# Kernel tuning notes

Hardware: AMD Instinct MI355X
Metric: run time of the kernel (lower is better)

Reference implementation:

```python
import jax, jax.numpy as jnp
import numpy as np

B, T, H, O, P, L = 128, 64, 512, 47, 4, 3
G = 4 * H


def setup_inputs() -> dict:
    key = jax.random.key(0)
    k = jax.random.split(key, 10)
    s = 0.05
    return {
        "x": jax.random.randint(k[0], (B, T), 0, O),
        "properties": jax.random.normal(k[1], (B, P), jnp.float32),
        "enc_w": jax.random.normal(k[2], (H, O), jnp.float32) * s,
        "enc_b": jnp.zeros((H,), jnp.float32),
        "dec_w": jax.random.normal(k[3], (O, H), jnp.float32) * s,
        "dec_b": jnp.zeros((O,), jnp.float32),
        "w_ih0": jax.random.normal(k[4], (G, H + P), jnp.float32) * s,
        "w_hh0": jax.random.normal(k[5], (G, H), jnp.float32) * s,
        "b_ih0": jnp.zeros((G,), jnp.float32).at[H:2 * H].set(1.0),
        "b_hh0": jnp.zeros((G,), jnp.float32).at[H:2 * H].set(1.0),
        "w_ih_rest": jax.random.normal(k[6], (L - 1, G, H), jnp.float32) * s,
        "w_hh_rest": jax.random.normal(k[7], (L - 1, G, H), jnp.float32) * s,
        "b_ih_rest": jnp.zeros((L - 1, G), jnp.float32).at[:, H:2 * H].set(1.0),
        "b_hh_rest": jnp.zeros((L - 1, G), jnp.float32).at[:, H:2 * H].set(1.0),
    }


def _lstm_cell(x, h, c, w_ih, w_hh, b_ih, b_hh):
    # torch gate order: i, f, g, o
    g = x @ w_ih.T + h @ w_hh.T + (b_ih + b_hh)
    i, f, gg, o = jnp.split(g, 4, axis=-1)
    c = jax.nn.sigmoid(f) * c + jax.nn.sigmoid(i) * jnp.tanh(gg)
    h = jax.nn.sigmoid(o) * jnp.tanh(c)
    return h, c


def reference(x, properties, enc_w, enc_b, dec_w, dec_b,
              w_ih0, w_hh0, b_ih0, b_hh0,
              w_ih_rest, w_hh_rest, b_ih_rest, b_hh_rest):
    batch = properties.shape[0]
    max_len = x.shape[1]
    n_layers = w_ih_rest.shape[0] + 1
    hidden = w_hh0.shape[1]
    out_size = dec_w.shape[0]

    # initial one-hot on symbol 1 (start token), encoded
    init = jnp.zeros((batch, out_size), properties.dtype).at[:, 1].set(1.0)
    inputs0 = init @ enc_w.T + enc_b  # [B, H]
    h0 = jnp.zeros((n_layers, batch, hidden), properties.dtype)
    c0 = jnp.zeros_like(h0)

    def step(carry, _):
        h, c, inp = carry
        xcat = jnp.concatenate([inp, properties], axis=1)  # [B, H+P]
        hs, cs = [], []
        hh, cc = _lstm_cell(xcat, h[0], c[0], w_ih0, w_hh0, b_ih0, b_hh0)
        hs.append(hh); cs.append(cc)
        for l in range(n_layers - 1):
            hh, cc = _lstm_cell(hh, h[l + 1], c[l + 1],
                                w_ih_rest[l], w_hh_rest[l],
                                b_ih_rest[l], b_hh_rest[l])
            hs.append(hh); cs.append(cc)
        logits = hh @ dec_w.T + dec_b          # [B, O]
        nxt = logits @ enc_w.T + enc_b         # feed logits back through encoder
        return (jnp.stack(hs), jnp.stack(cs), nxt), logits

    _, logits_seq = jax.lax.scan(step, (h0, c0, inputs0), None, length=max_len)
    return jnp.transpose(logits_seq, (1, 0, 2))  # [B, T, O]
```

## Files before the change

### kernel.cpp

```cpp
#include <hip/hip_runtime.h>
#include <hip/hip_fp16.h>
#include <math.h>

#define B 128
#define T 64
#define H 512
#define O 47
#define PP 4
#define G 2048
#define GH (G*H)
#define HB (H*B)


typedef _Float16 h16;
typedef _Float16 h16x2 __attribute__((ext_vector_type(2)));

__device__ __forceinline__ unsigned int pack2h(float a, float b) {
    union { unsigned int u; h16 h[2]; } c;
    c.h[0] = (h16)a; c.h[1] = (h16)b;
    return c.u;
}
__device__ __forceinline__ h16x2 as_h2(unsigned int u) {
    union { unsigned int u; h16x2 v; } c; c.u = u; return c.v;
}
__device__ __forceinline__ uint2 cload_u2(const unsigned int* p) {
    unsigned long long v = __hip_atomic_load((const unsigned long long*)p,
                                             __ATOMIC_RELAXED, __HIP_MEMORY_SCOPE_AGENT);
    union { unsigned long long u; uint2 w; } c; c.u = v; return c.w;
}
__device__ __forceinline__ void cstore_u2(unsigned int* p, uint2 v) {
    union { unsigned long long u; uint2 w; } c; c.w = v;
    __hip_atomic_store((unsigned long long*)p, c.u,
                       __ATOMIC_RELAXED, __HIP_MEMORY_SCOPE_AGENT);
}
#define FDOT2(w, x, c) __builtin_amdgcn_fdot2(as_h2(w), as_h2(x), (c), false)

#define SM_WH     0
#define SM_BIAS   12288
#define SM_DECH   14336
#define SM_BL     14592
#define SM_G      14608
#define SM_DB     22800
#define SM_H      23824
#define SM_TOTAL  24080

struct RnnParams {
  const float* w_hh0;
  const float* w_ihr;
  const float* w_hhr;
  const float* b_ihr;
  const float* b_hhr;
  const float* dec_w;
  const float* dec_b;
  const float* W0eff;
  const float* biasA;
  const float* biasB;
  unsigned int* h;
  float* c;
  float* out;
  unsigned int* arrive;
  unsigned int* gocnt;
};


__global__ __launch_bounds__(256) void k_init(
    const float* __restrict__ enc_w, const float* __restrict__ enc_b,
    const float* __restrict__ dec_b,
    float* __restrict__ h,
    float* __restrict__ c,
    float* __restrict__ d, float* __restrict__ nxt0,
    unsigned int* __restrict__ barptr)
{
    int idx = blockIdx.x * 256 + threadIdx.x;
    if (idx < 4160) barptr[idx] = 0u;
    #pragma unroll
    for (int i = 0; i < 3; ++i) h[i*HB + idx] = 0.f;
    #pragma unroll
    for (int i = 0; i < 3; ++i) c[i*HB + idx] = 0.f;
    if (idx < H) {
        float s = 0.f;
        for (int o = 0; o < O; ++o) s += enc_w[idx*O + o] * dec_b[o];
        d[idx] = enc_b[idx] + s;
        nxt0[idx] = enc_w[idx*O + 1] + enc_b[idx];
    }
}

__global__ __launch_bounds__(256) void k_M(
    const float* __restrict__ enc_w, const float* __restrict__ dec_w,
    float* __restrict__ M)
{
    int idx = blockIdx.x * 256 + threadIdx.x;
    int hh = idx >> 9, k = idx & 511;
    float s = 0.f;
    for (int o = 0; o < O; ++o) s += enc_w[hh*O + o] * dec_w[o*H + k];
    M[hh*H + k] = s;
}

__global__ __launch_bounds__(256) void k_cd(
    const float* __restrict__ w_ih0,
    const float* __restrict__ nxt0, const float* __restrict__ d,
    float* __restrict__ x0c, float* __restrict__ cd)
{
    int j = blockIdx.x * 256 + threadIdx.x;
    const float* row = w_ih0 + (size_t)j * (H + PP);
    float sA = 0.f, sB = 0.f;
    for (int k = 0; k < H; ++k) { float w = row[k]; sA += w * nxt0[k]; sB += w * d[k]; }
    x0c[j] = sA; cd[j] = sB;
}

__global__ __launch_bounds__(256) void k_W0eff(
    const float* __restrict__ w_ih0, const float* __restrict__ M,
    float* __restrict__ W0eff)
{
    int k0 = (threadIdx.x & 127) * 4;
    int jsub = threadIdx.x >> 7;
    int j0 = blockIdx.x * 16 + jsub * 8;
    float4 a[8];
    #pragma unroll
    for (int i = 0; i < 8; ++i) a[i] = make_float4(0.f, 0.f, 0.f, 0.f);
    for (int hh = 0; hh < H; ++hh) {
        float4 mv = *(const float4*)(M + (size_t)hh * H + k0);
        #pragma unroll
        for (int i = 0; i < 8; ++i) {
            float w = w_ih0[(size_t)(j0 + i) * (H + PP) + hh];
            a[i].x += w * mv.x; a[i].y += w * mv.y;
            a[i].z += w * mv.z; a[i].w += w * mv.w;
        }
    }
    #pragma unroll
    for (int i = 0; i < 8; ++i)
        *(float4*)(W0eff + (size_t)(j0 + i) * H + k0) = a[i];
}

__global__ __launch_bounds__(256) void k_bias(
    const float* __restrict__ w_ih0, const float* __restrict__ props,
    const float* __restrict__ b_ih0, const float* __restrict__ b_hh0,
    const float* __restrict__ x0c, const float* __restrict__ cd,
    float* __restrict__ biasA, float* __restrict__ biasB)
{
    int idx = blockIdx.x * 256 + threadIdx.x;
    int j = idx >> 7, b = idx & 127;
    const float* wp = w_ih0 + (size_t)j * (H + PP) + H;
    const float* pr = props + b * PP;
    float pc = wp[0]*pr[0] + wp[1]*pr[1] + wp[2]*pr[2] + wp[3]*pr[3];
    float base = b_ih0[j] + b_hh0[j] + pc;
    biasA[idx] = base + x0c[j];
    biasB[idx] = base + cd[j];
}


__global__ __launch_bounds__(512, 2) void rnn_persistent(RnnParams p)
{
    extern __shared__ float sm[];
    const int tid = threadIdx.x;
    const int wg  = blockIdx.x;
    const int u0  = wg * 2;
    const int b2  = tid & 63;
    const int ks  = tid >> 6;

    unsigned int* sWH   = (unsigned int*)(sm + SM_WH);
    float*        sBias = sm + SM_BIAS;
    unsigned int* sDecH = (unsigned int*)(sm + SM_DECH);
    float*        sBL   = sm + SM_BL;
    float2*       sGbuf = (float2*)(sm + SM_G);
    float2*       sDecb = (float2*)(sm + SM_DB);
    float*        sH    = sm + SM_H;

    unsigned int* h0p = p.h + 0*32768; unsigned int* h0c = p.h + 1*32768;
    unsigned int* h1p = p.h + 2*32768; unsigned int* h1c = p.h + 3*32768;
    unsigned int* h2p = p.h + 4*32768; unsigned int* h2c = p.h + 5*32768;
    float* c0 = p.c; float* c1 = p.c + HB; float* c2 = p.c + 2*HB;

    const bool  isdec = (wg < O);
    const float decb  = isdec ? p.dec_b[wg] : 0.f;

    auto stage = [&](int s, const float* base) {
        for (int idx = tid; idx < 2048; idx += 512) {
            int r = idx >> 8, kp = idx & 255;
            int j = (r >> 1) * H + u0 + (r & 1);
            const float* src = base + (size_t)j * H + 2*kp;
            sWH[s*2048 + (r << 8) + kp] = pack2h(src[0], src[1]);
        }
    };
    stage(0, p.W0eff);
    stage(1, p.w_hh0);
    stage(2, p.w_ihr);
    stage(3, p.w_hhr);
    stage(4, p.w_ihr + GH);
    stage(5, p.w_hhr + GH);
    for (int idx = tid; idx < 2048; idx += 512) {
        int pl = idx >> 10, r = (idx >> 7) & 7, b = idx & 127;
        int j = (r >> 1) * H + u0 + (r & 1);
        sBias[idx] = (pl ? p.biasB : p.biasA)[(size_t)j * B + b];
    }
    if (tid < 16) {
        int l = tid >> 3, r = tid & 7;
        int j = (r >> 1) * H + u0 + (r & 1);
        sBL[tid] = p.b_ihr[l*G + j] + p.b_hhr[l*G + j];
    }
    if (isdec && tid < 256) {
        const float* src = p.dec_w + (size_t)wg * H + 2*tid;
        sDecH[tid] = pack2h(src[0], src[1]);
    }
    __syncthreads();

    unsigned int epoch = 0;
    unsigned int* arrive = p.arrive;
    unsigned int* gocnt  = p.gocnt;

    auto gbar = [&]() {
        ++epoch;
        __syncthreads();
        if (tid == 0)
            __hip_atomic_fetch_add(&arrive[(size_t)wg * 16], 1u,
                                   __ATOMIC_RELEASE, __HIP_MEMORY_SCOPE_AGENT);
        if (wg == 0) {
            if (tid < 256) {
                while (__hip_atomic_load(&arrive[(size_t)tid * 16],
                        __ATOMIC_RELAXED, __HIP_MEMORY_SCOPE_AGENT) < epoch)
                    __builtin_amdgcn_s_sleep(1);
            }
            __syncthreads();
            if (tid == 0)
                __hip_atomic_fetch_add(gocnt, 1u,
                                       __ATOMIC_RELEASE, __HIP_MEMORY_SCOPE_AGENT);
        }
        if (tid == 0) {
            while (__hip_atomic_load(gocnt, __ATOMIC_RELAXED,
                                     __HIP_MEMORY_SCOPE_AGENT) < epoch)
                __builtin_amdgcn_s_sleep(1);
        }
        __syncthreads();
    };

    auto phase = [&](const unsigned int* __restrict__ xs,
                     const unsigned int* __restrict__ hs,
                     int ph, const float* biasPlane, const float* biasScal,
                     float* cc, unsigned int* hout, bool dopig, float* dout) {
        float2 acc[8];
        #pragma unroll
        for (int r = 0; r < 8; ++r) { acc[r].x = 0.f; acc[r].y = 0.f; }
        float2 accd; accd.x = 0.f; accd.y = 0.f;

        const unsigned int* wx = sWH + (ph*2 + 0) * 2048;
        const unsigned int* wh = sWH + (ph*2 + 1) * 2048;
        const int kb = ks * 32;
        const int xo = 2 * b2;

        if (dopig) {
            for (int kp = kb; kp < kb + 32; kp += 4) {
                uint2 x0 = cload_u2(xs + (kp+0)*128 + xo);
                uint2 x1 = cload_u2(xs + (kp+1)*128 + xo);
                uint2 x2 = cload_u2(xs + (kp+2)*128 + xo);
                uint2 x3 = cload_u2(xs + (kp+3)*128 + xo);
                uint4 dq = *(const uint4*)(sDecH + kp);
                accd.x = FDOT2(dq.x, x0.x, accd.x); accd.y = FDOT2(dq.x, x0.y, accd.y);
                accd.x = FDOT2(dq.y, x1.x, accd.x); accd.y = FDOT2(dq.y, x1.y, accd.y);
                accd.x = FDOT2(dq.z, x2.x, accd.x); accd.y = FDOT2(dq.z, x2.y, accd.y);
                accd.x = FDOT2(dq.w, x3.x, accd.x); accd.y = FDOT2(dq.w, x3.y, accd.y);
                #pragma unroll
                for (int r = 0; r < 8; ++r) {
                    uint4 wq = *(const uint4*)(wx + r*256 + kp);
                    acc[r].x = FDOT2(wq.x, x0.x, acc[r].x); acc[r].y = FDOT2(wq.x, x0.y, acc[r].y);
                    acc[r].x = FDOT2(wq.y, x1.x, acc[r].x); acc[r].y = FDOT2(wq.y, x1.y, acc[r].y);
                    acc[r].x = FDOT2(wq.z, x2.x, acc[r].x); acc[r].y = FDOT2(wq.z, x2.y, acc[r].y);
                    acc[r].x = FDOT2(wq.w, x3.x, acc[r].x); acc[r].y = FDOT2(wq.w, x3.y, acc[r].y);
                }
            }
        } else {
            for (int kp = kb; kp < kb + 32; kp += 4) {
                uint2 x0 = cload_u2(xs + (kp+0)*128 + xo);
                uint2 x1 = cload_u2(xs + (kp+1)*128 + xo);
                uint2 x2 = cload_u2(xs + (kp+2)*128 + xo);
                uint2 x3 = cload_u2(xs + (kp+3)*128 + xo);
                #pragma unroll
                for (int r = 0; r < 8; ++r) {
                    uint4 wq = *(const uint4*)(wx + r*256 + kp);
                    acc[r].x = FDOT2(wq.x, x0.x, acc[r].x); acc[r].y = FDOT2(wq.x, x0.y, acc[r].y);
                    acc[r].x = FDOT2(wq.y, x1.x, acc[r].x); acc[r].y = FDOT2(wq.y, x1.y, acc[r].y);
                    acc[r].x = FDOT2(wq.z, x2.x, acc[r].x); acc[r].y = FDOT2(wq.z, x2.y, acc[r].y);
                    acc[r].x = FDOT2(wq.w, x3.x, acc[r].x); acc[r].y = FDOT2(wq.w, x3.y, acc[r].y);
                }
            }
        }
        for (int kp = kb; kp < kb + 32; kp += 4) {
            uint2 x0 = cload_u2(hs + (kp+0)*128 + xo);
            uint2 x1 = cload_u2(hs + (kp+1)*128 + xo);
            uint2 x2 = cload_u2(hs + (kp+2)*128 + xo);
            uint2 x3 = cload_u2(hs + (kp+3)*128 + xo);
            #pragma unroll
            for (int r = 0; r < 8; ++r) {
                uint4 wq = *(const uint4*)(wh + r*256 + kp);
                acc[r].x = FDOT2(wq.x, x0.x, acc[r].x); acc[r].y = FDOT2(wq.x, x0.y, acc[r].y);
                acc[r].x = FDOT2(wq.y, x1.x, acc[r].x); acc[r].y = FDOT2(wq.y, x1.y, acc[r].y);
                acc[r].x = FDOT2(wq.z, x2.x, acc[r].x); acc[r].y = FDOT2(wq.z, x2.y, acc[r].y);
                acc[r].x = FDOT2(wq.w, x3.x, acc[r].x); acc[r].y = FDOT2(wq.w, x3.y, acc[r].y);
            }
        }

        #pragma unroll
        for (int r = 0; r < 8; ++r) sGbuf[(r*8 + ks)*64 + b2] = acc[r];
        if (dopig) sDecb[ks*64 + b2] = accd;
        __syncthreads();

        if (tid < 256) {
            int mi = tid >> 7, b = tid & 127;
            float g[4];
            #pragma unroll
            for (int q = 0; q < 4; ++q) {
                int r = q*2 + mi;
                float s = biasPlane ? biasPlane[r*128 + b] : biasScal[r];
                #pragma unroll
                for (int k2 = 0; k2 < 8; ++k2) {
                    float2 v = sGbuf[(r*8 + k2)*64 + (b >> 1)];
                    s += (b & 1) ? v.y : v.x;
                }
                g[q] = s;
            }
            float ig = 1.f/(1.f+expf(-g[0]));
            float fg = 1.f/(1.f+expf(-g[1]));
            float gv = tanhf(g[2]);
            float og = 1.f/(1.f+expf(-g[3]));
            int idx = (u0 + mi)*B + b;
            float cn = fg*cc[idx] + ig*gv;
            cc[idx] = cn;
            sH[mi*128 + b] = og*tanhf(cn);
        } else if (dopig && tid < 384) {
            int b = tid - 256;
            float s = decb;
            #pragma unroll
            for (int k2 = 0; k2 < 8; ++k2) {
                float2 v = sDecb[k2*64 + (b >> 1)];
                s += (b & 1) ? v.y : v.x;
            }
            dout[(size_t)b * (T*O)] = s;
        }
        __syncthreads();
        if (tid < 64) {
            int b0 = tid * 2;
            uint2 v;
            v.x = pack2h(sH[b0],     sH[128 + b0]);
            v.y = pack2h(sH[b0 + 1], sH[128 + b0 + 1]);
            cstore_u2(hout + wg*128 + b0, v);
        }
    };

    for (int t = 0; t < T; ++t) {
        bool pig = (t > 0) && isdec;
        phase(h2p, h0p, 0, sBias + (t == 0 ? 0 : 1024), nullptr,
              c0, h0c, pig, pig ? (p.out + (size_t)(t-1)*O + wg) : nullptr);
        gbar();
        phase(h0c, h1p, 1, nullptr, sBL, c1, h1c, false, nullptr);
        gbar();
        phase(h1c, h2p, 2, nullptr, sBL + 8, c2, h2c, false, nullptr);
        gbar();
        unsigned int* tp;
        tp = h0p; h0p = h0c; h0c = tp;
        tp = h1p; h1p = h1c; h1c = tp;
        tp = h2p; h2p = h2c; h2c = tp;
    }

    if (isdec) {
        float2 accd; accd.x = 0.f; accd.y = 0.f;
        const int kb = ks * 32;
        const int xo = 2 * b2;
        for (int kp = kb; kp < kb + 32; kp += 4) {
            uint2 x0 = cload_u2(h2p + (kp+0)*128 + xo);
            uint2 x1 = cload_u2(h2p + (kp+1)*128 + xo);
            uint2 x2 = cload_u2(h2p + (kp+2)*128 + xo);
            uint2 x3 = cload_u2(h2p + (kp+3)*128 + xo);
            uint4 dq = *(const uint4*)(sDecH + kp);
            accd.x = FDOT2(dq.x, x0.x, accd.x); accd.y = FDOT2(dq.x, x0.y, accd.y);
            accd.x = FDOT2(dq.y, x1.x, accd.x); accd.y = FDOT2(dq.y, x1.y, accd.y);
            accd.x = FDOT2(dq.z, x2.x, accd.x); accd.y = FDOT2(dq.z, x2.y, accd.y);
            accd.x = FDOT2(dq.w, x3.x, accd.x); accd.y = FDOT2(dq.w, x3.y, accd.y);
        }
        sDecb[ks*64 + b2] = accd;
    }
    __syncthreads();
    if (isdec && tid < 128) {
        int b = tid;
        float s = decb;
        #pragma unroll
        for (int k2 = 0; k2 < 8; ++k2) {
            float2 v = sDecb[k2*64 + (b >> 1)];
            s += (b & 1) ? v.y : v.x;
        }
        p.out[((size_t)b * T + 63) * O + wg] = s;
    }
}


__global__ __launch_bounds__(256) void init_kernel(
    const float* __restrict__ enc_w, const float* __restrict__ enc_b,
    float* __restrict__ nxtT, float* __restrict__ hbufs, float* __restrict__ cbufs)
{
    int idx = blockIdx.x * 256 + threadIdx.x;
    #pragma unroll
    for (int i = 0; i < 6; ++i) hbufs[i * HB + idx] = 0.f;
    #pragma unroll
    for (int i = 0; i < 3; ++i) cbufs[i * HB + idx] = 0.f;
    int h = idx >> 7;
    nxtT[idx] = enc_w[h * O + 1] + enc_b[h];
}

__global__ __launch_bounds__(256) void transpose_kernel(
    const float* __restrict__ dec_w, const float* __restrict__ enc_w,
    float* __restrict__ dec_wT, float* __restrict__ enc_wT)
{
    int idx = blockIdx.x * 256 + threadIdx.x;
    if (idx < O * H) {
        int o = idx / H, k = idx - o * H;
        dec_wT[k * O + o] = dec_w[o * H + k];
        enc_wT[o * H + k] = enc_w[k * O + o];
    }
}

__global__ __launch_bounds__(512) void gates_kernel(
    const float* __restrict__ xT, const float* __restrict__ hT,
    const float* __restrict__ w_ih, int ldih,
    const float* __restrict__ w_hh,
    const float* __restrict__ b_ih, const float* __restrict__ b_hh,
    const float* __restrict__ props,
    float* __restrict__ c, float* __restrict__ hout)
{
    const int wg = blockIdx.x;
    const int bg = wg >> 7, jg = wg & 127;
    const int m0 = jg * 4;
    const int lane_b = threadIdx.x & 63, ks = threadIdx.x >> 6;
    const int bb = (bg << 6) + lane_b;
    float acc[16];
    #pragma unroll
    for (int r = 0; r < 16; ++r) acc[r] = 0.f;
    const float* wih_rows[16]; const float* whh_rows[16];
    #pragma unroll
    for (int q = 0; q < 4; ++q)
        #pragma unroll
        for (int mi = 0; mi < 4; ++mi) {
            int r = q * 4 + mi, j = q * H + m0 + mi;
            wih_rows[r] = w_ih + (size_t)j * ldih;
            whh_rows[r] = w_hh + (size_t)j * H;
        }
    const int kbeg = ks * 64, kend = ks * 64 + 64;
    for (int k0 = kbeg; k0 < kend; k0 += 4) {
        float x0 = xT[(k0+0)*B+bb], x1 = xT[(k0+1)*B+bb];
        float x2 = xT[(k0+2)*B+bb], x3 = xT[(k0+3)*B+bb];
        #pragma unroll
        for (int r = 0; r < 16; ++r) {
            float4 wv = *(const float4*)(wih_rows[r] + k0);
            acc[r] += wv.x*x0 + wv.y*x1 + wv.z*x2 + wv.w*x3;
        }
    }
    for (int k0 = kbeg; k0 < kend; k0 += 4) {
        float x0 = hT[(k0+0)*B+bb], x1 = hT[(k0+1)*B+bb];
        float x2 = hT[(k0+2)*B+bb], x3 = hT[(k0+3)*B+bb];
        #pragma unroll
        for (int r = 0; r < 16; ++r) {
            float4 wv = *(const float4*)(whh_rows[r] + k0);
            acc[r] += wv.x*x0 + wv.y*x1 + wv.z*x2 + wv.w*x3;
        }
    }
    __shared__ float gbuf[16][8][64];
    #pragma unroll
    for (int r = 0; r < 16; ++r) gbuf[r][ks][lane_b] = acc[r];
    __syncthreads();
    if (threadIdx.x < 256) {
        int mi = threadIdx.x >> 6, b = threadIdx.x & 63;
        int bbo = (bg << 6) + b, m = m0 + mi;
        float g[4];
        #pragma unroll
        for (int q = 0; q < 4; ++q) {
            int j = q * H + m;
            float s = b_ih[j] + b_hh[j];
            #pragma unroll
            for (int k2 = 0; k2 < 8; ++k2) s += gbuf[q*4+mi][k2][b];
            if (props) {
                const float* wp = w_ih + (size_t)j * ldih + H;
                const float* pp = props + bbo * PP;
                s += wp[0]*pp[0] + wp[1]*pp[1] + wp[2]*pp[2] + wp[3]*pp[3];
            }
            g[q] = s;
        }
        float ig = 1.f/(1.f+expf(-g[0]));
        float fg = 1.f/(1.f+expf(-g[1]));
        float gv = tanhf(g[2]);
        float og = 1.f/(1.f+expf(-g[3]));
        int idx = m * B + bbo;
        float cn = fg * c[idx] + ig * gv;
        c[idx] = cn;
        hout[idx] = og * tanhf(cn);
    }
}

__global__ __launch_bounds__(256) void decenc_kernel(
    const float* __restrict__ h2T, const float* __restrict__ dec_wT,
    const float* __restrict__ dec_b, const float* __restrict__ enc_wT,
    const float* __restrict__ enc_b, float* __restrict__ nxtT,
    float* __restrict__ out, int t)
{
    const int b = blockIdx.x;
    const int w = threadIdx.x >> 6, o = threadIdx.x & 63;
    __shared__ float red[4][64];
    __shared__ float lg[64];
    float p = 0.f;
    if (o < O)
        for (int k = w * 128; k < w * 128 + 128; ++k)
            p += h2T[k * B + b] * dec_wT[k * O + o];
    red[w][o] = p;
    __syncthreads();
    if (threadIdx.x < 64) {
        int oo = threadIdx.x;
        float s = 0.f;
        if (oo < O) {
            s = dec_b[oo] + red[0][oo] + red[1][oo] + red[2][oo] + red[3][oo];
            out[((size_t)b * T + t) * O + oo] = s;
        }
        lg[oo] = s;
    }
    __syncthreads();
    for (int h = threadIdx.x; h < H; h += 256) {
        float s = enc_b[h];
        #pragma unroll 1
        for (int oo = 0; oo < O; ++oo) s += lg[oo] * enc_wT[oo * H + h];
        nxtT[h * B + b] = s;
    }
}

extern "C" void kernel_launch(void* const* d_in, const int* in_sizes, int n_in,
                              void* d_out, int out_size, void* d_ws, size_t ws_size,
                              hipStream_t stream) {
    const float* props = (const float*)d_in[1];
    const float* enc_w = (const float*)d_in[2];
    const float* enc_b = (const float*)d_in[3];
    const float* dec_w = (const float*)d_in[4];
    const float* dec_b = (const float*)d_in[5];
    const float* w_ih0 = (const float*)d_in[6];
    const float* w_hh0 = (const float*)d_in[7];
    const float* b_ih0 = (const float*)d_in[8];
    const float* b_hh0 = (const float*)d_in[9];
    const float* w_ihr = (const float*)d_in[10];
    const float* w_hhr = (const float*)d_in[11];
    const float* b_ihr = (const float*)d_in[12];
    const float* b_hhr = (const float*)d_in[13];

    float* ws = (float*)d_ws;
    const size_t NEED = ((size_t)34 * HB + 5120 + 4160) * sizeof(float);
    const size_t LDS_BYTES = (size_t)SM_TOTAL * sizeof(float);

    static int lds_attr_set = -1;
    if (lds_attr_set < 0) {
        lds_attr_set = (hipFuncSetAttribute((const void*)rnn_persistent,
                         hipFuncAttributeMaxDynamicSharedMemorySize,
                         (int)LDS_BYTES) == hipSuccess) ? 1 : 0;
    }

    if (ws_size >= NEED && lds_attr_set == 1) {
        unsigned int* hbuf = (unsigned int*)ws;
        float* cbuf  = ws + 3*HB;
        float* M     = ws + 6*HB;
        float* W0eff = ws + 10*HB;
        float* biasA = ws + 26*HB;
        float* biasB = ws + 30*HB;
        float* dvec  = ws + 34*HB;
        float* nxt0  = dvec + 512;
        float* x0c   = nxt0 + 512;
        float* cd    = x0c + 2048;
        unsigned int* barptr = (unsigned int*)(cd + 2048);

        k_init<<<256, 256, 0, stream>>>(enc_w, enc_b, dec_b, (float*)hbuf, cbuf,
                                        dvec, nxt0, barptr);
        k_M<<<1024, 256, 0, stream>>>(enc_w, dec_w, M);
        k_cd<<<8, 256, 0, stream>>>(w_ih0, nxt0, dvec, x0c, cd);
        k_W0eff<<<128, 256, 0, stream>>>(w_ih0, M, W0eff);
        k_bias<<<1024, 256, 0, stream>>>(w_ih0, props, b_ih0, b_hh0, x0c, cd, biasA, biasB);

        RnnParams prm;
        prm.w_hh0 = w_hh0; prm.w_ihr = w_ihr; prm.w_hhr = w_hhr;
        prm.b_ihr = b_ihr; prm.b_hhr = b_hhr;
        prm.dec_w = dec_w; prm.dec_b = dec_b;
        prm.W0eff = W0eff; prm.biasA = biasA; prm.biasB = biasB;
        prm.h = hbuf; prm.c = cbuf; prm.out = (float*)d_out;
        prm.arrive = barptr; prm.gocnt = barptr + 4096;

        void* args[] = { &prm };
        hipLaunchCooperativeKernel((const void*)rnn_persistent,
                                   dim3(256), dim3(512), args,
                                   (unsigned int)LDS_BYTES, stream);
        return;
    }

    float* nxtT   = ws;
    float* hb     = ws + HB;
    float* cb     = ws + 7*HB;
    float* dec_wT = ws + 10*HB;
    float* enc_wT = dec_wT + H*O;

    init_kernel<<<256, 256, 0, stream>>>(enc_w, enc_b, nxtT, hb, cb);
    transpose_kernel<<<(O*H + 255)/256, 256, 0, stream>>>(dec_w, enc_w, dec_wT, enc_wT);

    float* hprev[3]; float* hcur[3];
    for (int l = 0; l < 3; ++l) { hprev[l] = hb + (2*l)*HB; hcur[l] = hb + (2*l+1)*HB; }

    for (int t = 0; t < T; ++t) {
        gates_kernel<<<256, 512, 0, stream>>>(nxtT, hprev[0], w_ih0, H+PP, w_hh0,
                                              b_ih0, b_hh0, props, cb, hcur[0]);
        gates_kernel<<<256, 512, 0, stream>>>(hcur[0], hprev[1], w_ihr, H, w_hhr,
                                              b_ihr, b_hhr, nullptr, cb + HB, hcur[1]);
        gates_kernel<<<256, 512, 0, stream>>>(hcur[1], hprev[2], w_ihr + (size_t)G*H, H,
                                              w_hhr + (size_t)G*H, b_ihr + G, b_hhr + G,
                                              nullptr, cb + 2*HB, hcur[2]);
        decenc_kernel<<<B, 256, 0, stream>>>(hcur[2], dec_wT, dec_b, enc_wT, enc_b,
                                             nxtT, (float*)d_out, t);
        for (int l = 0; l < 3; ++l) { float* tp = hprev[l]; hprev[l] = hcur[l]; hcur[l] = tp; }
    }
}
```

Measured before the change: 2.452 ms.

## Use per-timestep h slots with plain vector loads and wider per-thread batch tiles

```diff
diff --git a/kernel.cpp b/kernel.cpp
--- a/kernel.cpp
+++ b/kernel.cpp
@@ -43,6 +43,18 @@
 #define SM_DB     22800
 #define SM_H      23824
 #define SM_TOTAL  24080
+
+#define HSLOT   32768
+#define NSLOT   65
+#define HTOT    (3 * NSLOT * HSLOT)
+#define OFF_C   HTOT
+#define OFF_M   (OFF_C + 3*HB)
+#define OFF_W0  (OFF_M + 4*HB)
+#define OFF_BA  (OFF_W0 + 16*HB)
+#define OFF_BB  (OFF_BA + 4*HB)
+#define OFF_DV  (OFF_BB + 4*HB)
+#define OFF_BAR (OFF_DV + 5120)
+#define NEED_A  ((size_t)(OFF_BAR + 4160) * sizeof(float))
 
 struct RnnParams {
   const float* w_hh0;
@@ -63,11 +75,33 @@
 };
 
 
-__global__ __launch_bounds__(256) void k_init(
+__global__ __launch_bounds__(256) void k_init_a(
     const float* __restrict__ enc_w, const float* __restrict__ enc_b,
     const float* __restrict__ dec_b,
-    float* __restrict__ h,
-    float* __restrict__ c,
+    unsigned int* __restrict__ h, float* __restrict__ c,
+    float* __restrict__ d, float* __restrict__ nxt0,
+    unsigned int* __restrict__ barptr)
+{
+    int idx = blockIdx.x * 256 + threadIdx.x;
+    if (idx < 4160) barptr[idx] = 0u;
+    if (idx < HSLOT) {
+        #pragma unroll
+        for (int l = 0; l < 3; ++l) h[(size_t)l * NSLOT * HSLOT + idx] = 0u;
+    }
+    #pragma unroll
+    for (int i = 0; i < 3; ++i) c[i*HB + idx] = 0.f;
+    if (idx < H) {
+        float s = 0.f;
+        for (int o = 0; o < O; ++o) s += enc_w[idx*O + o] * dec_b[o];
+        d[idx] = enc_b[idx] + s;
+        nxt0[idx] = enc_w[idx*O + 1] + enc_b[idx];
+    }
+}
+
+__global__ __launch_bounds__(256) void k_init_b(
+    const float* __restrict__ enc_w, const float* __restrict__ enc_b,
+    const float* __restrict__ dec_b,
+    float* __restrict__ h, float* __restrict__ c,
     float* __restrict__ d, float* __restrict__ nxt0,
     unsigned int* __restrict__ barptr)
 {
@@ -149,59 +183,63 @@
 }
 
 
-__global__ __launch_bounds__(512, 2) void rnn_persistent(RnnParams p)
+__device__ __forceinline__ void stage_weights(
+    unsigned int* sWH, float* sBias, unsigned int* sDecH, float* sBL,
+    const RnnParams& p, int wg, int u0, int tid, bool isdec)
+{
+    const float* bases[6] = { p.W0eff, p.w_hh0, p.w_ihr, p.w_hhr,
+                              p.w_ihr + GH, p.w_hhr + GH };
+    #pragma unroll
+    for (int s = 0; s < 6; ++s) {
+        for (int idx = tid; idx < 2048; idx += 512) {
+            int r = idx >> 8, kp = idx & 255;
+            int j = (r >> 1) * H + u0 + (r & 1);
+            const float* src = bases[s] + (size_t)j * H + 2*kp;
+            sWH[s*2048 + (r << 8) + kp] = pack2h(src[0], src[1]);
+        }
+    }
+    for (int idx = tid; idx < 2048; idx += 512) {
+        int pl = idx >> 10, r = (idx >> 7) & 7, b = idx & 127;
+        int j = (r >> 1) * H + u0 + (r & 1);
+        sBias[idx] = (pl ? p.biasB : p.biasA)[(size_t)j * B + b];
+    }
+    if (tid < 16) {
+        int l = tid >> 3, r = tid & 7;
+        int j = (r >> 1) * H + u0 + (r & 1);
+        sBL[tid] = p.b_ihr[l*G + j] + p.b_hhr[l*G + j];
+    }
+    if (isdec && tid < 256) {
+        const float* src = p.dec_w + (size_t)wg * H + 2*tid;
+        sDecH[tid] = pack2h(src[0], src[1]);
+    }
+}
+
+
+__global__ __launch_bounds__(512, 2) void rnn_persistent_a(RnnParams p)
 {
     extern __shared__ float sm[];
-    const int tid = threadIdx.x;
-    const int wg  = blockIdx.x;
-    const int u0  = wg * 2;
-    const int b2  = tid & 63;
-    const int ks  = tid >> 6;
+    const int tid   = threadIdx.x;
+    const int wg    = blockIdx.x;
+    const int u0    = wg * 2;
+    const int b4    = tid & 31;
+    const int khalf = (tid >> 5) & 1;
+    const int ks    = tid >> 6;
 
     unsigned int* sWH   = (unsigned int*)(sm + SM_WH);
     float*        sBias = sm + SM_BIAS;
     unsigned int* sDecH = (unsigned int*)(sm + SM_DECH);
     float*        sBL   = sm + SM_BL;
-    float2*       sGbuf = (float2*)(sm + SM_G);
-    float2*       sDecb = (float2*)(sm + SM_DB);
+    float*        sG    = sm + SM_G;
+    float*        sDb   = sm + SM_DB;
     float*        sH    = sm + SM_H;
 
-    unsigned int* h0p = p.h + 0*32768; unsigned int* h0c = p.h + 1*32768;
-    unsigned int* h1p = p.h + 2*32768; unsigned int* h1c = p.h + 3*32768;
-    unsigned int* h2p = p.h + 4*32768; unsigned int* h2c = p.h + 5*32768;
     float* c0 = p.c; float* c1 = p.c + HB; float* c2 = p.c + 2*HB;
-
     const bool  isdec = (wg < O);
     const float decb  = isdec ? p.dec_b[wg] : 0.f;
 
-    auto stage = [&](int s, const float* base) {
-        for (int idx = tid; idx < 2048; idx += 512) {
-            int r = idx >> 8, kp = idx & 255;
-            int j = (r >> 1) * H + u0 + (r & 1);
-            const float* src = base + (size_t)j * H + 2*kp;
-            sWH[s*2048 + (r << 8) + kp] = pack2h(src[0], src[1]);
-        }
-    };
-    stage(0, p.W0eff);
-    stage(1, p.w_hh0);
-    stage(2, p.w_ihr);
-    stage(3, p.w_hhr);
-    stage(4, p.w_ihr + GH);
-    stage(5, p.w_hhr + GH);
-    for (int idx = tid; idx < 2048; idx += 512) {
-        int pl = idx >> 10, r = (idx >> 7) & 7, b = idx & 127;
-        int j = (r >> 1) * H + u0 + (r & 1);
-        sBias[idx] = (pl ? p.biasB : p.biasA)[(size_t)j * B + b];
-    }
-    if (tid < 16) {
-        int l = tid >> 3, r = tid & 7;
-        int j = (r >> 1) * H + u0 + (r & 1);
-        sBL[tid] = p.b_ihr[l*G + j] + p.b_hhr[l*G + j];
-    }
-    if (isdec && tid < 256) {
-        const float* src = p.dec_w + (size_t)wg * H + 2*tid;
-        sDecH[tid] = pack2h(src[0], src[1]);
-    }
+    __builtin_amdgcn_fence(__ATOMIC_ACQUIRE, "agent");
+
+    stage_weights(sWH, sBias, sDecH, sBL, p, wg, u0, tid, isdec);
     __syncthreads();
 
     unsigned int epoch = 0;
@@ -233,6 +271,239 @@
         __syncthreads();
     };
 
+    auto slot = [&](int l, int s) -> unsigned int* {
+        return p.h + ((size_t)(l * NSLOT + s) << 15);
+    };
+
+    auto phase = [&](const unsigned int* __restrict__ xs,
+                     const unsigned int* __restrict__ hs,
+                     int ph, const float* biasPlane, const float* biasScal,
+                     float* cc, unsigned int* hout, bool dopig, float* dout) {
+        float4 acc[8];
+        #pragma unroll
+        for (int r = 0; r < 8; ++r) acc[r] = make_float4(0.f, 0.f, 0.f, 0.f);
+        float4 accd = make_float4(0.f, 0.f, 0.f, 0.f);
+
+        const unsigned int* wx = sWH + (ph*2 + 0) * 2048;
+        const unsigned int* wh = sWH + (ph*2 + 1) * 2048;
+        const int kp0 = ks * 32 + khalf * 16;
+        const int xo  = 4 * b4;
+
+        for (int kp = kp0; kp < kp0 + 16; kp += 4) {
+            uint4 x0 = *(const uint4*)(xs + (kp+0)*128 + xo);
+            uint4 x1 = *(const uint4*)(xs + (kp+1)*128 + xo);
+            uint4 x2 = *(const uint4*)(xs + (kp+2)*128 + xo);
+            uint4 x3 = *(const uint4*)(xs + (kp+3)*128 + xo);
+            #pragma unroll
+            for (int r = 0; r < 8; ++r) {
+                uint4 wq = *(const uint4*)(wx + r*256 + kp);
+                acc[r].x = FDOT2(wq.x, x0.x, acc[r].x); acc[r].y = FDOT2(wq.x, x0.y, acc[r].y);
+                acc[r].z = FDOT2(wq.x, x0.z, acc[r].z); acc[r].w = FDOT2(wq.x, x0.w, acc[r].w);
+                acc[r].x = FDOT2(wq.y, x1.x, acc[r].x); acc[r].y = FDOT2(wq.y, x1.y, acc[r].y);
+                acc[r].z = FDOT2(wq.y, x1.z, acc[r].z); acc[r].w = FDOT2(wq.y, x1.w, acc[r].w);
+                acc[r].x = FDOT2(wq.z, x2.x, acc[r].x); acc[r].y = FDOT2(wq.z, x2.y, acc[r].y);
+                acc[r].z = FDOT2(wq.z, x2.z, acc[r].z); acc[r].w = FDOT2(wq.z, x2.w, acc[r].w);
+                acc[r].x = FDOT2(wq.w, x3.x, acc[r].x); acc[r].y = FDOT2(wq.w, x3.y, acc[r].y);
+                acc[r].z = FDOT2(wq.w, x3.z, acc[r].z); acc[r].w = FDOT2(wq.w, x3.w, acc[r].w);
+            }
+            if (dopig) {
+                uint4 dq = *(const uint4*)(sDecH + kp);
+                accd.x = FDOT2(dq.x, x0.x, accd.x); accd.y = FDOT2(dq.x, x0.y, accd.y);
+                accd.z = FDOT2(dq.x, x0.z, accd.z); accd.w = FDOT2(dq.x, x0.w, accd.w);
+                accd.x = FDOT2(dq.y, x1.x, accd.x); accd.y = FDOT2(dq.y, x1.y, accd.y);
+                accd.z = FDOT2(dq.y, x1.z, accd.z); accd.w = FDOT2(dq.y, x1.w, accd.w);
+                accd.x = FDOT2(dq.z, x2.x, accd.x); accd.y = FDOT2(dq.z, x2.y, accd.y);
+                accd.z = FDOT2(dq.z, x2.z, accd.z); accd.w = FDOT2(dq.z, x2.w, accd.w);
+                accd.x = FDOT2(dq.w, x3.x, accd.x); accd.y = FDOT2(dq.w, x3.y, accd.y);
+                accd.z = FDOT2(dq.w, x3.z, accd.z); accd.w = FDOT2(dq.w, x3.w, accd.w);
+            }
+        }
+        for (int kp = kp0; kp < kp0 + 16; kp += 4) {
+            uint4 x0 = *(const uint4*)(hs + (kp+0)*128 + xo);
+            uint4 x1 = *(const uint4*)(hs + (kp+1)*128 + xo);
+            uint4 x2 = *(const uint4*)(hs + (kp+2)*128 + xo);
+            uint4 x3 = *(const uint4*)(hs + (kp+3)*128 + xo);
+            #pragma unroll
+            for (int r = 0; r < 8; ++r) {
+                uint4 wq = *(const uint4*)(wh + r*256 + kp);
+                acc[r].x = FDOT2(wq.x, x0.x, acc[r].x); acc[r].y = FDOT2(wq.x, x0.y, acc[r].y);
+                acc[r].z = FDOT2(wq.x, x0.z, acc[r].z); acc[r].w = FDOT2(wq.x, x0.w, acc[r].w);
+                acc[r].x = FDOT2(wq.y, x1.x, acc[r].x); acc[r].y = FDOT2(wq.y, x1.y, acc[r].y);
+                acc[r].z = FDOT2(wq.y, x1.z, acc[r].z); acc[r].w = FDOT2(wq.y, x1.w, acc[r].w);
+                acc[r].x = FDOT2(wq.z, x2.x, acc[r].x); acc[r].y = FDOT2(wq.z, x2.y, acc[r].y);
+                acc[r].z = FDOT2(wq.z, x2.z, acc[r].z); acc[r].w = FDOT2(wq.z, x2.w, acc[r].w);
+                acc[r].x = FDOT2(wq.w, x3.x, acc[r].x); acc[r].y = FDOT2(wq.w, x3.y, acc[r].y);
+                acc[r].z = FDOT2(wq.w, x3.z, acc[r].z); acc[r].w = FDOT2(wq.w, x3.w, acc[r].w);
+            }
+        }
+
+        #pragma unroll
+        for (int r = 0; r < 8; ++r) {
+            acc[r].x += __shfl_xor(acc[r].x, 32, 64);
+            acc[r].y += __shfl_xor(acc[r].y, 32, 64);
+            acc[r].z += __shfl_xor(acc[r].z, 32, 64);
+            acc[r].w += __shfl_xor(acc[r].w, 32, 64);
+        }
+        if (khalf == 0) {
+            #pragma unroll
+            for (int r = 0; r < 8; ++r)
+                *(float4*)(sG + ((r*8 + ks)*32 + b4)*4) = acc[r];
+        }
+        if (dopig) {
+            accd.x += __shfl_xor(accd.x, 32, 64);
+            accd.y += __shfl_xor(accd.y, 32, 64);
+            accd.z += __shfl_xor(accd.z, 32, 64);
+            accd.w += __shfl_xor(accd.w, 32, 64);
+            if (khalf == 0) *(float4*)(sDb + (ks*32 + b4)*4) = accd;
+        }
+        __syncthreads();
+
+        if (tid < 256) {
+            int mi = tid >> 7, b = tid & 127;
+            float g[4];
+            #pragma unroll
+            for (int q = 0; q < 4; ++q) {
+                int r = q*2 + mi;
+                float s = biasPlane ? biasPlane[r*128 + b] : biasScal[r];
+                #pragma unroll
+                for (int k2 = 0; k2 < 8; ++k2)
+                    s += sG[((r*8 + k2)*32 + (b >> 2))*4 + (b & 3)];
+                g[q] = s;
+            }
+            float ig = 1.f/(1.f+expf(-g[0]));
+            float fg = 1.f/(1.f+expf(-g[1]));
+            float gv = tanhf(g[2]);
+            float og = 1.f/(1.f+expf(-g[3]));
+            int idx = (u0 + mi)*B + b;
+            float cn = fg*cc[idx] + ig*gv;
+            cc[idx] = cn;
+            sH[mi*128 + b] = og*tanhf(cn);
+        } else if (dopig && tid < 384) {
+            int b = tid - 256;
+            float s = decb;
+            #pragma unroll
+            for (int k2 = 0; k2 < 8; ++k2)
+                s += sDb[(k2*32 + (b >> 2))*4 + (b & 3)];
+            dout[(size_t)b * (T*O)] = s;
+        }
+        __syncthreads();
+        if (tid < 64) {
+            int b0 = tid * 2;
+            uint2 v;
+            v.x = pack2h(sH[b0],     sH[128 + b0]);
+            v.y = pack2h(sH[b0 + 1], sH[128 + b0 + 1]);
+            cstore_u2(hout + wg*128 + b0, v);
+        }
+    };
+
+    for (int t = 0; t < T; ++t) {
+        bool pig = (t > 0) && isdec;
+        phase(slot(2, t), slot(0, t), 0, sBias + (t == 0 ? 0 : 1024), nullptr,
+              c0, slot(0, t+1), pig,
+              pig ? (p.out + (size_t)(t-1)*O + wg) : nullptr);
+        gbar();
+        phase(slot(0, t+1), slot(1, t), 1, nullptr, sBL, c1, slot(1, t+1),
+              false, nullptr);
+        gbar();
+        phase(slot(1, t+1), slot(2, t), 2, nullptr, sBL + 8, c2, slot(2, t+1),
+              false, nullptr);
+        gbar();
+    }
+
+    if (isdec) {
+        const unsigned int* xs = slot(2, T);
+        float4 accd = make_float4(0.f, 0.f, 0.f, 0.f);
+        const int kp0 = ks * 32 + khalf * 16;
+        const int xo  = 4 * b4;
+        for (int kp = kp0; kp < kp0 + 16; kp += 4) {
+            uint4 x0 = *(const uint4*)(xs + (kp+0)*128 + xo);
+            uint4 x1 = *(const uint4*)(xs + (kp+1)*128 + xo);
+            uint4 x2 = *(const uint4*)(xs + (kp+2)*128 + xo);
+            uint4 x3 = *(const uint4*)(xs + (kp+3)*128 + xo);
+            uint4 dq = *(const uint4*)(sDecH + kp);
+            accd.x = FDOT2(dq.x, x0.x, accd.x); accd.y = FDOT2(dq.x, x0.y, accd.y);
+            accd.z = FDOT2(dq.x, x0.z, accd.z); accd.w = FDOT2(dq.x, x0.w, accd.w);
+            accd.x = FDOT2(dq.y, x1.x, accd.x); accd.y = FDOT2(dq.y, x1.y, accd.y);
+            accd.z = FDOT2(dq.y, x1.z, accd.z); accd.w = FDOT2(dq.y, x1.w, accd.w);
+            accd.x = FDOT2(dq.z, x2.x, accd.x); accd.y = FDOT2(dq.z, x2.y, accd.y);
+            accd.z = FDOT2(dq.z, x2.z, accd.z); accd.w = FDOT2(dq.z, x2.w, accd.w);
+            accd.x = FDOT2(dq.w, x3.x, accd.x); accd.y = FDOT2(dq.w, x3.y, accd.y);
+            accd.z = FDOT2(dq.w, x3.z, accd.z); accd.w = FDOT2(dq.w, x3.w, accd.w);
+        }
+        accd.x += __shfl_xor(accd.x, 32, 64);
+        accd.y += __shfl_xor(accd.y, 32, 64);
+        accd.z += __shfl_xor(accd.z, 32, 64);
+        accd.w += __shfl_xor(accd.w, 32, 64);
+        if (khalf == 0) *(float4*)(sDb + (ks*32 + b4)*4) = accd;
+    }
+    __syncthreads();
+    if (isdec && tid < 128) {
+        int b = tid;
+        float s = decb;
+        #pragma unroll
+        for (int k2 = 0; k2 < 8; ++k2)
+            s += sDb[(k2*32 + (b >> 2))*4 + (b & 3)];
+        p.out[((size_t)b * T + 63) * O + wg] = s;
+    }
+}
+
+
+__global__ __launch_bounds__(512, 2) void rnn_persistent_b(RnnParams p)
+{
+    extern __shared__ float sm[];
+    const int tid = threadIdx.x;
+    const int wg  = blockIdx.x;
+    const int u0  = wg * 2;
+    const int b2  = tid & 63;
+    const int ks  = tid >> 6;
+
+    unsigned int* sWH   = (unsigned int*)(sm + SM_WH);
+    float*        sBias = sm + SM_BIAS;
+    unsigned int* sDecH = (unsigned int*)(sm + SM_DECH);
+    float*        sBL   = sm + SM_BL;
+    float2*       sGbuf = (float2*)(sm + SM_G);
+    float2*       sDecb = (float2*)(sm + SM_DB);
+    float*        sH    = sm + SM_H;
+
+    unsigned int* h0p = p.h + 0*32768; unsigned int* h0c = p.h + 1*32768;
+    unsigned int* h1p = p.h + 2*32768; unsigned int* h1c = p.h + 3*32768;
+    unsigned int* h2p = p.h + 4*32768; unsigned int* h2c = p.h + 5*32768;
+    float* c0 = p.c; float* c1 = p.c + HB; float* c2 = p.c + 2*HB;
+
+    const bool  isdec = (wg < O);
+    const float decb  = isdec ? p.dec_b[wg] : 0.f;
+
+    stage_weights(sWH, sBias, sDecH, sBL, p, wg, u0, tid, isdec);
+    __syncthreads();
+
+    unsigned int epoch = 0;
+    unsigned int* arrive = p.arrive;
+    unsigned int* gocnt  = p.gocnt;
+    auto gbar = [&]() {
+        ++epoch;
+        __syncthreads();
+        if (tid == 0)
+            __hip_atomic_fetch_add(&arrive[(size_t)wg * 16], 1u,
+                                   __ATOMIC_RELEASE, __HIP_MEMORY_SCOPE_AGENT);
+        if (wg == 0) {
+            if (tid < 256) {
+                while (__hip_atomic_load(&arrive[(size_t)tid * 16],
+                        __ATOMIC_RELAXED, __HIP_MEMORY_SCOPE_AGENT) < epoch)
+                    __builtin_amdgcn_s_sleep(1);
+            }
+            __syncthreads();
+            if (tid == 0)
+                __hip_atomic_fetch_add(gocnt, 1u,
+                                       __ATOMIC_RELEASE, __HIP_MEMORY_SCOPE_AGENT);
+        }
+        if (tid == 0) {
+            while (__hip_atomic_load(gocnt, __ATOMIC_RELAXED,
+                                     __HIP_MEMORY_SCOPE_AGENT) < epoch)
+                __builtin_amdgcn_s_sleep(1);
+        }
+        __syncthreads();
+    };
+
     auto phase = [&](const unsigned int* __restrict__ xs,
                      const unsigned int* __restrict__ hs,
                      int ph, const float* biasPlane, const float* biasScal,
@@ -247,40 +518,25 @@
         const int kb = ks * 32;
         const int xo = 2 * b2;
 
-        if (dopig) {
-            for (int kp = kb; kp < kb + 32; kp += 4) {
-                uint2 x0 = cload_u2(xs + (kp+0)*128 + xo);
-                uint2 x1 = cload_u2(xs + (kp+1)*128 + xo);
-                uint2 x2 = cload_u2(xs + (kp+2)*128 + xo);
-                uint2 x3 = cload_u2(xs + (kp+3)*128 + xo);
+        for (int kp = kb; kp < kb + 32; kp += 4) {
+            uint2 x0 = cload_u2(xs + (kp+0)*128 + xo);
+            uint2 x1 = cload_u2(xs + (kp+1)*128 + xo);
+            uint2 x2 = cload_u2(xs + (kp+2)*128 + xo);
+            uint2 x3 = cload_u2(xs + (kp+3)*128 + xo);
+            if (dopig) {
                 uint4 dq = *(const uint4*)(sDecH + kp);
                 accd.x = FDOT2(dq.x, x0.x, accd.x); accd.y = FDOT2(dq.x, x0.y, accd.y);
                 accd.x = FDOT2(dq.y, x1.x, accd.x); accd.y = FDOT2(dq.y, x1.y, accd.y);
                 accd.x = FDOT2(dq.z, x2.x, accd.x); accd.y = FDOT2(dq.z, x2.y, accd.y);
                 accd.x = FDOT2(dq.w, x3.x, accd.x); accd.y = FDOT2(dq.w, x3.y, accd.y);
-                #pragma unroll
-                for (int r = 0; r < 8; ++r) {
-                    uint4 wq = *(const uint4*)(wx + r*256 + kp);
-                    acc[r].x = FDOT2(wq.x, x0.x, acc[r].x); acc[r].y = FDOT2(wq.x, x0.y, acc[r].y);
-                    acc[r].x = FDOT2(wq.y, x1.x, acc[r].x); acc[r].y = FDOT2(wq.y, x1.y, acc[r].y);
-                    acc[r].x = FDOT2(wq.z, x2.x, acc[r].x); acc[r].y = FDOT2(wq.z, x2.y, acc[r].y);
-                    acc[r].x = FDOT2(wq.w, x3.x, acc[r].x); acc[r].y = FDOT2(wq.w, x3.y, acc[r].y);
-                }
-            }
-        } else {
-            for (int kp = kb; kp < kb + 32; kp += 4) {
-                uint2 x0 = cload_u2(xs + (kp+0)*128 + xo);
-                uint2 x1 = cload_u2(xs + (kp+1)*128 + xo);
-                uint2 x2 = cload_u2(xs + (kp+2)*128 + xo);
-                uint2 x3 = cload_u2(xs + (kp+3)*128 + xo);
-                #pragma unroll
-                for (int r = 0; r < 8; ++r) {
-                    uint4 wq = *(const uint4*)(wx + r*256 + kp);
-                    acc[r].x = FDOT2(wq.x, x0.x, acc[r].x); acc[r].y = FDOT2(wq.x, x0.y, acc[r].y);
-                    acc[r].x = FDOT2(wq.y, x1.x, acc[r].x); acc[r].y = FDOT2(wq.y, x1.y, acc[r].y);
-                    acc[r].x = FDOT2(wq.z, x2.x, acc[r].x); acc[r].y = FDOT2(wq.z, x2.y, acc[r].y);
-                    acc[r].x = FDOT2(wq.w, x3.x, acc[r].x); acc[r].y = FDOT2(wq.w, x3.y, acc[r].y);
-                }
+            }
+            #pragma unroll
+            for (int r = 0; r < 8; ++r) {
+                uint4 wq = *(const uint4*)(wx + r*256 + kp);
+                acc[r].x = FDOT2(wq.x, x0.x, acc[r].x); acc[r].y = FDOT2(wq.x, x0.y, acc[r].y);
+                acc[r].x = FDOT2(wq.y, x1.x, acc[r].x); acc[r].y = FDOT2(wq.y, x1.y, acc[r].y);
+                acc[r].x = FDOT2(wq.z, x2.x, acc[r].x); acc[r].y = FDOT2(wq.z, x2.y, acc[r].y);
+                acc[r].x = FDOT2(wq.w, x3.x, acc[r].x); acc[r].y = FDOT2(wq.w, x3.y, acc[r].y);
             }
         }
         for (int kp = kb; kp < kb + 32; kp += 4) {
@@ -544,17 +800,56 @@
     const float* b_hhr = (const float*)d_in[13];
 
     float* ws = (float*)d_ws;
-    const size_t NEED = ((size_t)34 * HB + 5120 + 4160) * sizeof(float);
+    const size_t NEED_B = ((size_t)34 * HB + 5120 + 4160) * sizeof(float);
     const size_t LDS_BYTES = (size_t)SM_TOTAL * sizeof(float);
 
-    static int lds_attr_set = -1;
-    if (lds_attr_set < 0) {
-        lds_attr_set = (hipFuncSetAttribute((const void*)rnn_persistent,
-                         hipFuncAttributeMaxDynamicSharedMemorySize,
-                         (int)LDS_BYTES) == hipSuccess) ? 1 : 0;
-    }
-
-    if (ws_size >= NEED && lds_attr_set == 1) {
+    static int lds_a = -1, lds_b = -1;
+    if (lds_a < 0) {
+        lds_a = (hipFuncSetAttribute((const void*)rnn_persistent_a,
+                  hipFuncAttributeMaxDynamicSharedMemorySize,
+                  (int)LDS_BYTES) == hipSuccess) ? 1 : 0;
+        lds_b = (hipFuncSetAttribute((const void*)rnn_persistent_b,
+                  hipFuncAttributeMaxDynamicSharedMemorySize,
+                  (int)LDS_BYTES) == hipSuccess) ? 1 : 0;
+    }
+
+    if (ws_size >= NEED_A && lds_a == 1) {
+        unsigned int* hbuf = (unsigned int*)ws;
+        float* cbuf  = ws + OFF_C;
+        float* M     = ws + OFF_M;
+        float* W0eff = ws + OFF_W0;
+        float* biasA = ws + OFF_BA;
+        float* biasB = ws + OFF_BB;
+        float* dvec  = ws + OFF_DV;
+        float* nxt0  = dvec + 512;
+        float* x0c   = nxt0 + 512;
+        float* cd    = x0c + 2048;
+        unsigned int* barptr = (unsigned int*)(ws + OFF_BAR);
+
+        k_init_a<<<256, 256, 0, stream>>>(enc_w, enc_b, dec_b, hbuf, cbuf,
+                                          dvec, nxt0, barptr);
+        k_M<<<1024, 256, 0, stream>>>(enc_w, dec_w, M);
+        k_cd<<<8, 256, 0, stream>>>(w_ih0, nxt0, dvec, x0c, cd);
+        k_W0eff<<<128, 256, 0, stream>>>(w_ih0, M, W0eff);
+        k_bias<<<1024, 256, 0, stream>>>(w_ih0, props, b_ih0, b_hh0, x0c, cd,
+                                         biasA, biasB);
+
+        RnnParams prm;
+        prm.w_hh0 = w_hh0; prm.w_ihr = w_ihr; prm.w_hhr = w_hhr;
+        prm.b_ihr = b_ihr; prm.b_hhr = b_hhr;
+        prm.dec_w = dec_w; prm.dec_b = dec_b;
+        prm.W0eff = W0eff; prm.biasA = biasA; prm.biasB = biasB;
+        prm.h = hbuf; prm.c = cbuf; prm.out = (float*)d_out;
+        prm.arrive = barptr; prm.gocnt = barptr + 4096;
+
+        void* args[] = { &prm };
+        hipLaunchCooperativeKernel((const void*)rnn_persistent_a,
+                                   dim3(256), dim3(512), args,
+                                   (unsigned int)LDS_BYTES, stream);
+        return;
+    }
+
+    if (ws_size >= NEED_B && lds_b == 1) {
         unsigned int* hbuf = (unsigned int*)ws;
         float* cbuf  = ws + 3*HB;
         float* M     = ws + 6*HB;
@@ -567,12 +862,13 @@
         float* cd    = x0c + 2048;
         unsigned int* barptr = (unsigned int*)(cd + 2048);
 
-        k_init<<<256, 256, 0, stream>>>(enc_w, enc_b, dec_b, (float*)hbuf, cbuf,
-                                        dvec, nxt0, barptr);
+        k_init_b<<<256, 256, 0, stream>>>(enc_w, enc_b, dec_b, (float*)hbuf,
+                                          cbuf, dvec, nxt0, barptr);
         k_M<<<1024, 256, 0, stream>>>(enc_w, dec_w, M);
         k_cd<<<8, 256, 0, stream>>>(w_ih0, nxt0, dvec, x0c, cd);
         k_W0eff<<<128, 256, 0, stream>>>(w_ih0, M, W0eff);
-        k_bias<<<1024, 256, 0, stream>>>(w_ih0, props, b_ih0, b_hh0, x0c, cd, biasA, biasB);
+        k_bias<<<1024, 256, 0, stream>>>(w_ih0, props, b_ih0, b_hh0, x0c, cd,
+                                         biasA, biasB);
 
         RnnParams prm;
         prm.w_hh0 = w_hh0; prm.w_ihr = w_ihr; prm.w_hhr = w_hhr;
@@ -583,7 +879,7 @@
         prm.arrive = barptr; prm.gocnt = barptr + 4096;
 
         void* args[] = { &prm };
-        hipLaunchCooperativeKernel((const void*)rnn_persistent,
+        hipLaunchCooperativeKernel((const void*)rnn_persistent_b,
                                    dim3(256), dim3(512), args,
                                    (unsigned int)LDS_BYTES, stream);
         return;
```

Measured after the change: 2.323 ms. -5.2%, faster.
